# Kernel optimization log

Measured on AMD Instinct MI355X. Metric: run time of the kernel, lower is better.

The kernel has to match this reference:

```python
import jax, jax.numpy as jnp
import numpy as np
from jax import lax

LATENT = 64
NUM_EMB = 512
BETA = 0.25
DN = ('NCHW', 'OIHW', 'NCHW')


def conv(x, w, b, stride, pad):
    y = lax.conv_general_dilated(x, w, (stride, stride), [(pad, pad), (pad, pad)],
                                 dimension_numbers=DN)
    return y + b[None, :, None, None]


def tconv(x, w, b, stride, pad, opad):
    # torch ConvTranspose2d(k=3, stride, padding=pad, output_padding=opad)
    # == dilated conv with lhs_dilation=stride, padding (k-1-pad, k-1-pad+opad),
    #    spatially-flipped kernel. w is stored OIHW (out, in, kh, kw).
    k = w.shape[2]
    lo, hi = k - 1 - pad, k - 1 - pad + opad
    y = lax.conv_general_dilated(x, w[:, :, ::-1, ::-1], (1, 1), [(lo, hi), (lo, hi)],
                                 lhs_dilation=(stride, stride), dimension_numbers=DN)
    return y + b[None, :, None, None]


def vector_quantize(z, codebook):
    # z: (B, D, H, W); codebook: (K, D)
    B, D, H, W = z.shape
    flat = z.transpose(0, 2, 3, 1).reshape(-1, D)  # (BHW, D)
    d = (jnp.sum(flat ** 2, axis=1, keepdims=True)
         + jnp.sum(codebook ** 2, axis=1)
         - 2.0 * flat @ codebook.T)  # (BHW, K)
    idx = jnp.argmin(d, axis=1)
    q = codebook[idx].reshape(B, H, W, D).transpose(0, 3, 1, 2)  # (B, D, H, W)
    commitment = jnp.mean((lax.stop_gradient(q) - z) ** 2)
    codebook_loss = jnp.mean((q - lax.stop_gradient(z)) ** 2)
    loss = BETA * commitment + codebook_loss
    q_ste = z + lax.stop_gradient(q - z)  # straight-through estimator
    return q_ste, loss


def setup_inputs() -> dict:
    key = jax.random.key(0)
    ks = jax.random.split(key, 16)
    f32 = jnp.float32
    inp = {
        'x': jax.random.uniform(ks[0], (1024, 1, 50, 50), dtype=f32),
        'enc_w1': jax.random.normal(ks[1], (32, 1, 3, 3), f32) * 0.1,
        'enc_b1': jnp.zeros((32,), f32),
        'enc_w2': jax.random.normal(ks[2], (64, 32, 3, 3), f32) * 0.05,
        'enc_b2': jnp.zeros((64,), f32),
        'enc_w3': jax.random.normal(ks[3], (LATENT, 64, 1, 1), f32) * 0.1,
        'enc_b3': jnp.zeros((LATENT,), f32),
        'codebook': jax.random.uniform(ks[4], (NUM_EMB, LATENT), dtype=f32),
        'dec_w1': jax.random.normal(ks[5], (64, LATENT, 3, 3), f32) * 0.05,
        'dec_b1': jnp.zeros((64,), f32),
        'dec_w2': jax.random.normal(ks[6], (32, 64, 3, 3), f32) * 0.05,
        'dec_b2': jnp.zeros((32,), f32),
        'dec_w3': jax.random.normal(ks[7], (1, 32, 3, 3), f32) * 0.05,
        'dec_b3': jnp.zeros((1,), f32),
    }
    return inp


def reference(x, enc_w1, enc_b1, enc_w2, enc_b2, enc_w3, enc_b3, codebook,
              dec_w1, dec_b1, dec_w2, dec_b2, dec_w3, dec_b3):
    # encoder: (B,1,50,50) -> (B,LATENT,13,13)
    h = jax.nn.relu(conv(x, enc_w1, enc_b1, 2, 1))
    h = jax.nn.relu(conv(h, enc_w2, enc_b2, 2, 1))
    z = conv(h, enc_w3, enc_b3, 1, 0)
    q, vq_loss = vector_quantize(z, codebook)
    # decoder: 13 -> 25 -> 50
    h = jax.nn.relu(tconv(q, dec_w1, dec_b1, 2, 1, 0))
    h = jax.nn.relu(tconv(h, dec_w2, dec_b2, 2, 1, 1))
    x_recon = jax.nn.sigmoid(conv(h, dec_w3, dec_b3, 1, 1))
    return x_recon, vq_loss
```

## Files before the change

### kernel.cpp

```cpp
#include <hip/hip_runtime.h>
#include <math.h>


typedef __attribute__((ext_vector_type(8))) short s8v;
typedef __attribute__((ext_vector_type(4))) float f4v;
typedef __attribute__((ext_vector_type(4))) int i4v;
typedef __attribute__((ext_vector_type(4))) short s4v;
typedef __attribute__((ext_vector_type(2))) float f2v;

__device__ inline unsigned short f2bf(float f) {
    unsigned u = __builtin_bit_cast(unsigned, f);
    return (unsigned short)((u + 0x7fffu + ((u >> 16) & 1u)) >> 16);
}
__device__ inline float bf2f(unsigned short h) {
    return __builtin_bit_cast(float, ((unsigned)h) << 16);
}

__global__ __launch_bounds__(256) void k_prep_all(
        const float* __restrict__ cb,  const float* __restrict__ ew2,
        const float* __restrict__ ew3, const float* __restrict__ dw1,
        const float* __restrict__ dw2, const float* __restrict__ dw3,
        unsigned short* __restrict__ cbm, unsigned short* __restrict__ wB2n,
        unsigned short* __restrict__ wB1, unsigned short* __restrict__ wB2,
        unsigned short* __restrict__ wB3, float* __restrict__ cn,
        float* __restrict__ loss, f2v* __restrict__ wpk) {
    int i = blockIdx.x * 256 + threadIdx.x;
    if (i < 98304) {
        int j = i & 7, lane = (i >> 3) & 63;
        int kc = (i >> 9) % 6, nt = (i >> 9) / 6;
        int n = nt * 16 + (lane & 15);
        int k = kc * 32 + ((lane >> 4) << 3) + j;
        int seg = k >> 6, kk = k & 63;
        float c = cb[n * 64 + kk];
        unsigned short ch = f2bf(c);
        cbm[i] = (seg == 1) ? f2bf(c - bf2f(ch)) : ch;
    } else if (i < 153600) {
        int q = i - 98304;
        int j = q & 7, lane = (q >> 3) & 63;
        int kc = (q >> 9) % 27, nt = (q >> 9) / 27;
        int k = kc * 32 + ((lane >> 4) << 3) + j;
        int co = nt * 16 + (lane & 15);
        int part = (k < 288) ? 0 : (k < 576) ? 1 : 0;
        int kk = (k < 288) ? k : (k < 576) ? k - 288 : k - 576;
        int tap = kk >> 5, ci = kk & 31;
        float v = ew2[(co * 32 + ci) * 9 + tap];
        unsigned short hi = f2bf(v);
        wB2n[q] = part ? f2bf(v - bf2f(hi)) : hi;
    } else if (i < 219136) {
        int q = i - 153600;
        int j = q & 7, l = (q >> 3) & 63, kc = (q >> 9) & 7, nt = q >> 12;
        int n = nt * 16 + (l & 15), k = kc * 32 + (l >> 4) * 8 + j;
        int cls = n >> 6, co = n & 63, p = k >> 6, ci = k & 63;
        int jh = -1, jw = -1;
        if (cls == 0)      { if (p == 0) { jh = 1; jw = 1; } }
        else if (cls == 1) { if (p == 1) { jh = 1; jw = 0; } else if (p == 0) { jh = 1; jw = 2; } }
        else if (cls == 2) { if (p == 2) { jh = 0; jw = 1; } else if (p == 0) { jh = 2; jw = 1; } }
        else { if (p == 3) { jh = 0; jw = 0; } else if (p == 2) { jh = 0; jw = 2; }
               else if (p == 1) { jh = 2; jw = 0; } else { jh = 2; jw = 2; } }
        float v = (jh >= 0) ? dw1[((co * 64 + ci) * 3 + jh) * 3 + jw] : 0.f;
        wB1[q] = f2bf(v);
    } else if (i < 251904) {
        int q = i - 219136;
        int j = q & 7, l = (q >> 3) & 63, kc = (q >> 9) & 7, nt = q >> 12;
        int n = nt * 16 + (l & 15), k = kc * 32 + (l >> 4) * 8 + j;
        int cls = n >> 5, co = n & 31, p = k >> 6, ci = k & 63;
        int jh = -1, jw = -1;
        if (cls == 0)      { if (p == 0) { jh = 1; jw = 1; } }
        else if (cls == 1) { if (p == 1) { jh = 1; jw = 0; } else if (p == 0) { jh = 1; jw = 2; } }
        else if (cls == 2) { if (p == 2) { jh = 0; jw = 1; } else if (p == 0) { jh = 2; jw = 1; } }
        else { if (p == 3) { jh = 0; jw = 0; } else if (p == 2) { jh = 0; jw = 2; }
               else if (p == 1) { jh = 2; jw = 0; } else { jh = 2; jw = 2; } }
        float v = (jh >= 0) ? dw2[((co * 64 + ci) * 3 + jh) * 3 + jw] : 0.f;
        wB2[q] = f2bf(v);
    } else if (i < 264192) {
        int q = i - 251904;
        int j = q & 7, lane = (q >> 3) & 63;
        int kc = (q >> 9) % 6, nt = (q >> 9) / 6;
        int k = kc * 32 + ((lane >> 4) << 3) + j;
        int n = nt * 16 + (lane & 15);
        int part = (k < 64) ? 0 : (k < 128) ? 1 : 0;
        int kk = (k < 64) ? k : (k < 128) ? k - 64 : k - 128;
        float v = ew3[n * 64 + kk];
        unsigned short hi = f2bf(v);
        wB3[q] = part ? f2bf(v - bf2f(hi)) : hi;
    } else if (i < 264704) {
        int k = i - 264192;
        const float* r = cb + k * 64;
        float s = 0.f;
#pragma unroll
        for (int c = 0; c < 64; ++c) s += r[c] * r[c];
        cn[k] = s;
    } else if (i == 264704) {
        *loss = 0.f;
    } else if (i < 264849) {
        int q = i - 264705;
        int kw = q / 48, rem = q % 48, kh = rem / 16, ii = rem % 16;
        f2v w;
        w[0] = dw3[(2 * ii) * 9 + kh * 3 + kw];
        w[1] = dw3[(2 * ii + 1) * 9 + kh * 3 + kw];
        wpk[q] = w;
    }
}

__global__ __launch_bounds__(256) void k_conv1(const float* __restrict__ x,
                                               const float* __restrict__ w,
                                               const float* __restrict__ b,
                                               unsigned short* __restrict__ h1,
                                               int total) {
    __shared__ float4 wl4[72];
    float* wl = (float*)wl4;
    int tid = threadIdx.x;
    for (int t = tid; t < 288; t += 256) {
        int tap = t >> 5, co = t & 31;
        wl[t] = w[co * 9 + tap];
    }
    __syncthreads();
    int pix = blockIdx.x * 256 + tid;
    if (pix >= total) return;
    int n = pix / 625, p = pix % 625, oh = p / 25, ow = p % 25;
    const float* xp = x + (size_t)n * 2500;
    float4 a[8];
#pragma unroll
    for (int j = 0; j < 8; ++j) a[j] = ((const float4*)b)[j];
#pragma unroll
    for (int kh = 0; kh < 3; ++kh) {
        int ih = 2 * oh - 1 + kh;
        if ((unsigned)ih >= 50u) continue;
#pragma unroll
        for (int kw = 0; kw < 3; ++kw) {
            int iw = 2 * ow - 1 + kw;
            if ((unsigned)iw >= 50u) continue;
            float v = xp[ih * 50 + iw];
            int tap = kh * 3 + kw;
#pragma unroll
            for (int j = 0; j < 8; ++j) {
                float4 ww = wl4[tap * 8 + j];
                a[j].x += v * ww.x; a[j].y += v * ww.y;
                a[j].z += v * ww.z; a[j].w += v * ww.w;
            }
        }
    }
    unsigned short hi[32], lo[32];
#pragma unroll
    for (int j = 0; j < 8; ++j) {
        float vv[4] = {a[j].x, a[j].y, a[j].z, a[j].w};
#pragma unroll
        for (int e = 0; e < 4; ++e) {
            float v = fmaxf(vv[e], 0.f);
            unsigned short h = f2bf(v);
            hi[j * 4 + e] = h;
            lo[j * 4 + e] = f2bf(v - bf2f(h));
        }
    }
    i4v* op = (i4v*)(h1 + (size_t)pix * 64);
#pragma unroll
    for (int g = 0; g < 4; ++g) {
        i4v ph, pl;
#pragma unroll
        for (int e = 0; e < 4; ++e) {
            int b0 = g * 8 + e * 2;
            ph[e] = (int)((unsigned)hi[b0] | ((unsigned)hi[b0 + 1] << 16));
            pl[e] = (int)((unsigned)lo[b0] | ((unsigned)lo[b0 + 1] << 16));
        }
        op[g] = ph;
        op[4 + g] = pl;
    }
}

__global__ __launch_bounds__(256, 2) void k_enc_m(const unsigned short* __restrict__ h1,
                                                  const unsigned short* __restrict__ B2n,
                                                  const unsigned short* __restrict__ B3,
                                                  const float* __restrict__ b2,
                                                  const float* __restrict__ b3,
                                                  unsigned short* __restrict__ z, int npix) {
    __shared__ short a1[16 * 728];
    __shared__ short a2[16 * 136];
    __shared__ short czs[16 * 136];
    int tid = threadIdx.x, blk = blockIdx.x;
#pragma unroll
    for (int pass = 0; pass < 5; ++pass) {
        int u = tid + pass * 256;
        if (u < 1152) {
            int m = u / 72, rem = u - m * 72;
            int idx = rem >> 2, sub = rem & 3;
            int seg = (idx >= 9) ? 1 : 0;
            int t = idx - seg * 9;
            i4v v = (i4v){0, 0, 0, 0};
            int pix = blk * 16 + m;
            if (pix < npix) {
                int n = pix / 169, p = pix % 169, oh = p / 13, ow = p % 13;
                int ih = 2 * oh - 1 + t / 3, iw = 2 * ow - 1 + t % 3;
                if (((unsigned)ih < 25u) && ((unsigned)iw < 25u))
                    v = *(const i4v*)(h1 + (((size_t)n * 25 + ih) * 25 + iw) * 64
                                      + (seg * 4 + sub) * 8);
            }
            *(i4v*)(a1 + m * 728 + seg * 360 + t * 40 + sub * 8) = v;
        }
    }
    __syncthreads();
    int wave = tid >> 6, lane = tid & 63;
    int r = lane & 15, g = lane >> 4;
    int abase = r * 728 + g * 8;
    s8v ah[9], al[9];
#pragma unroll
    for (int t = 0; t < 9; ++t) {
        ah[t] = *(const s8v*)(a1 + abase + t * 40);
        al[t] = *(const s8v*)(a1 + abase + 360 + t * 40);
    }
    f4v acc = (f4v){0.f, 0.f, 0.f, 0.f};
#pragma unroll
    for (int kc = 0; kc < 27; ++kc) {
        s8v b = *(const s8v*)((const short*)B2n + ((size_t)((wave * 27 + kc) * 64 + lane)) * 8);
        s8v a = (kc < 9) ? ah[kc] : (kc < 18) ? ah[kc - 9] : al[kc - 18];
        acc = __builtin_amdgcn_mfma_f32_16x16x32_bf16(a, b, acc, 0, 0, 0);
    }
    {
        float bv = b2[wave * 16 + r];
        int n = wave * 16 + r;
#pragma unroll
        for (int rr = 0; rr < 4; ++rr) {
            int m = g * 4 + rr;
            float h = fmaxf(acc[rr] + bv, 0.f);
            unsigned short hh = f2bf(h);
            a2[m * 136 + n] = (short)hh;
            a2[m * 136 + 64 + n] = (short)f2bf(h - bf2f(hh));
        }
    }
    __syncthreads();
    int arow2 = r * 136 + g * 8;
    s8v zh0 = *(const s8v*)(a2 + arow2);
    s8v zh1 = *(const s8v*)(a2 + arow2 + 32);
    s8v zl0 = *(const s8v*)(a2 + arow2 + 64);
    s8v zl1 = *(const s8v*)(a2 + arow2 + 96);
    f4v acc2 = (f4v){0.f, 0.f, 0.f, 0.f};
    {
        const short* bp3 = (const short*)B3 + ((size_t)(wave * 6 * 64 + lane)) * 8;
        s8v b0 = *(const s8v*)(bp3);
        s8v b1 = *(const s8v*)(bp3 + 64 * 8);
        s8v b2f = *(const s8v*)(bp3 + 2 * 64 * 8);
        s8v b3f = *(const s8v*)(bp3 + 3 * 64 * 8);
        s8v b4 = *(const s8v*)(bp3 + 4 * 64 * 8);
        s8v b5 = *(const s8v*)(bp3 + 5 * 64 * 8);
        acc2 = __builtin_amdgcn_mfma_f32_16x16x32_bf16(zh0, b0, acc2, 0, 0, 0);
        acc2 = __builtin_amdgcn_mfma_f32_16x16x32_bf16(zh1, b1, acc2, 0, 0, 0);
        acc2 = __builtin_amdgcn_mfma_f32_16x16x32_bf16(zh0, b2f, acc2, 0, 0, 0);
        acc2 = __builtin_amdgcn_mfma_f32_16x16x32_bf16(zh1, b3f, acc2, 0, 0, 0);
        acc2 = __builtin_amdgcn_mfma_f32_16x16x32_bf16(zl0, b4, acc2, 0, 0, 0);
        acc2 = __builtin_amdgcn_mfma_f32_16x16x32_bf16(zl1, b5, acc2, 0, 0, 0);
    }
    {
        float bv = b3[wave * 16 + r];
        int n = wave * 16 + r;
#pragma unroll
        for (int rr = 0; rr < 4; ++rr) {
            int m = g * 4 + rr;
            float v = acc2[rr] + bv;
            unsigned short hh = f2bf(v);
            czs[m * 136 + n] = (short)hh;
            czs[m * 136 + 64 + n] = (short)f2bf(v - bf2f(hh));
        }
    }
    __syncthreads();
    {
        int m = tid >> 4, t = tid & 15;
        int pix = blk * 16 + m;
        if (pix < npix)
            *(i4v*)(z + (size_t)pix * 128 + t * 8) = *(i4v*)(czs + m * 136 + t * 8);
    }
}

__global__ __launch_bounds__(256, 2) void k_vq_m(const unsigned short* __restrict__ z,
                                                 const float* __restrict__ cb,
                                                 const unsigned short* __restrict__ cbm,
                                                 const float* __restrict__ cn,
                                                 unsigned short* __restrict__ q,
                                                 float* __restrict__ lpart, int npix) {
    __shared__ short a_lds[128 * 136];
    __shared__ int bkf[128];
    __shared__ float lred4[4];
    int tid = threadIdx.x, blk = blockIdx.x;
    {
        const i4v* src = (const i4v*)(z + (size_t)blk * 128 * 128);
#pragma unroll
        for (int it = 0; it < 8; ++it) {
            int L = it * 256 + tid;
            int m = L >> 4, s = L & 15;
            int pix = blk * 128 + m;
            i4v v = (i4v){0, 0, 0, 0};
            if (pix < npix) v = src[L];
            *(i4v*)(a_lds + m * 136 + s * 8) = v;
        }
    }
    __syncthreads();
    int wave = tid >> 6, lane = tid & 63;
    int arow0 = (wave * 32 + (lane & 15)) * 136 + (lane >> 4) * 8;
    int arow1 = arow0 + 16 * 136;
    s8v af00 = *(const s8v*)(a_lds + arow0);
    s8v af01 = *(const s8v*)(a_lds + arow0 + 32);
    s8v af02 = *(const s8v*)(a_lds + arow0 + 64);
    s8v af03 = *(const s8v*)(a_lds + arow0 + 96);
    s8v af10 = *(const s8v*)(a_lds + arow1);
    s8v af11 = *(const s8v*)(a_lds + arow1 + 32);
    s8v af12 = *(const s8v*)(a_lds + arow1 + 64);
    s8v af13 = *(const s8v*)(a_lds + arow1 + 96);
    float bd0[4], bd1[4];
    int bk0[4], bk1[4];
#pragma unroll
    for (int r = 0; r < 4; ++r) {
        bd0[r] = 3.4e38f; bk0[r] = 0;
        bd1[r] = 3.4e38f; bk1[r] = 0;
    }
    const s8v* bp = (const s8v*)cbm + lane;
    int ln15 = lane & 15;
    s8v bfA[6], bfB[6];
#pragma unroll
    for (int kc = 0; kc < 6; ++kc) bfA[kc] = bp[kc * 64];
    float cnA = cn[ln15];
    float cnB;
    for (int nt = 0; nt < 32; nt += 2) {
#pragma unroll
        for (int kc = 0; kc < 6; ++kc) bfB[kc] = bp[((nt + 1) * 6 + kc) * 64];
        cnB = cn[(nt + 1) * 16 + ln15];
        {
            f4v acc0 = (f4v){0.f, 0.f, 0.f, 0.f};
            f4v acc1 = (f4v){0.f, 0.f, 0.f, 0.f};
            acc0 = __builtin_amdgcn_mfma_f32_16x16x32_bf16(af00, bfA[0], acc0, 0, 0, 0);
            acc1 = __builtin_amdgcn_mfma_f32_16x16x32_bf16(af10, bfA[0], acc1, 0, 0, 0);
            acc0 = __builtin_amdgcn_mfma_f32_16x16x32_bf16(af01, bfA[1], acc0, 0, 0, 0);
            acc1 = __builtin_amdgcn_mfma_f32_16x16x32_bf16(af11, bfA[1], acc1, 0, 0, 0);
            acc0 = __builtin_amdgcn_mfma_f32_16x16x32_bf16(af00, bfA[2], acc0, 0, 0, 0);
            acc1 = __builtin_amdgcn_mfma_f32_16x16x32_bf16(af10, bfA[2], acc1, 0, 0, 0);
            acc0 = __builtin_amdgcn_mfma_f32_16x16x32_bf16(af01, bfA[3], acc0, 0, 0, 0);
            acc1 = __builtin_amdgcn_mfma_f32_16x16x32_bf16(af11, bfA[3], acc1, 0, 0, 0);
            acc0 = __builtin_amdgcn_mfma_f32_16x16x32_bf16(af02, bfA[4], acc0, 0, 0, 0);
            acc1 = __builtin_amdgcn_mfma_f32_16x16x32_bf16(af12, bfA[4], acc1, 0, 0, 0);
            acc0 = __builtin_amdgcn_mfma_f32_16x16x32_bf16(af03, bfA[5], acc0, 0, 0, 0);
            acc1 = __builtin_amdgcn_mfma_f32_16x16x32_bf16(af13, bfA[5], acc1, 0, 0, 0);
            int kcol = nt * 16 + ln15;
#pragma unroll
            for (int r = 0; r < 4; ++r) {
                float d0 = cnA - 2.f * acc0[r];
                if (d0 < bd0[r]) { bd0[r] = d0; bk0[r] = kcol; }
                float d1 = cnA - 2.f * acc1[r];
                if (d1 < bd1[r]) { bd1[r] = d1; bk1[r] = kcol; }
            }
        }
        if (nt + 2 < 32) {
#pragma unroll
            for (int kc = 0; kc < 6; ++kc) bfA[kc] = bp[((nt + 2) * 6 + kc) * 64];
            cnA = cn[(nt + 2) * 16 + ln15];
        }
        {
            f4v acc0 = (f4v){0.f, 0.f, 0.f, 0.f};
            f4v acc1 = (f4v){0.f, 0.f, 0.f, 0.f};
            acc0 = __builtin_amdgcn_mfma_f32_16x16x32_bf16(af00, bfB[0], acc0, 0, 0, 0);
            acc1 = __builtin_amdgcn_mfma_f32_16x16x32_bf16(af10, bfB[0], acc1, 0, 0, 0);
            acc0 = __builtin_amdgcn_mfma_f32_16x16x32_bf16(af01, bfB[1], acc0, 0, 0, 0);
            acc1 = __builtin_amdgcn_mfma_f32_16x16x32_bf16(af11, bfB[1], acc1, 0, 0, 0);
            acc0 = __builtin_amdgcn_mfma_f32_16x16x32_bf16(af00, bfB[2], acc0, 0, 0, 0);
            acc1 = __builtin_amdgcn_mfma_f32_16x16x32_bf16(af10, bfB[2], acc1, 0, 0, 0);
            acc0 = __builtin_amdgcn_mfma_f32_16x16x32_bf16(af01, bfB[3], acc0, 0, 0, 0);
            acc1 = __builtin_amdgcn_mfma_f32_16x16x32_bf16(af11, bfB[3], acc1, 0, 0, 0);
            acc0 = __builtin_amdgcn_mfma_f32_16x16x32_bf16(af02, bfB[4], acc0, 0, 0, 0);
            acc1 = __builtin_amdgcn_mfma_f32_16x16x32_bf16(af12, bfB[4], acc1, 0, 0, 0);
            acc0 = __builtin_amdgcn_mfma_f32_16x16x32_bf16(af03, bfB[5], acc0, 0, 0, 0);
            acc1 = __builtin_amdgcn_mfma_f32_16x16x32_bf16(af13, bfB[5], acc1, 0, 0, 0);
            int kcol = (nt + 1) * 16 + ln15;
#pragma unroll
            for (int r = 0; r < 4; ++r) {
                float d0 = cnB - 2.f * acc0[r];
                if (d0 < bd0[r]) { bd0[r] = d0; bk0[r] = kcol; }
                float d1 = cnB - 2.f * acc1[r];
                if (d1 < bd1[r]) { bd1[r] = d1; bk1[r] = kcol; }
            }
        }
    }
#pragma unroll
    for (int off = 1; off < 16; off <<= 1) {
#pragma unroll
        for (int r = 0; r < 4; ++r) {
            float od = __shfl_xor(bd0[r], off);
            int ok = __shfl_xor(bk0[r], off);
            if (od < bd0[r] || (od == bd0[r] && ok < bk0[r])) { bd0[r] = od; bk0[r] = ok; }
            od = __shfl_xor(bd1[r], off);
            ok = __shfl_xor(bk1[r], off);
            if (od < bd1[r] || (od == bd1[r] && ok < bk1[r])) { bd1[r] = od; bk1[r] = ok; }
        }
    }
    if ((lane & 15) == 0) {
#pragma unroll
        for (int r = 0; r < 4; ++r) {
            bkf[wave * 32 + (lane >> 4) * 4 + r] = bk0[r];
            bkf[wave * 32 + 16 + (lane >> 4) * 4 + r] = bk1[r];
        }
    }
    __syncthreads();
    float lsum = 0.f;
#pragma unroll
    for (int it = 0; it < 8; ++it) {
        int L = it * 256 + tid;
        int m = L >> 4, c4 = L & 15;
        int pix = blk * 128 + m;
        if (pix < npix) {
            int k0 = bkf[m];
            float4 cq = ((const float4*)cb)[(size_t)k0 * 16 + c4];
            const short* rz = a_lds + m * 136 + c4 * 4;
            s4v zh4 = *(const s4v*)rz;
            s4v zl4 = *(const s4v*)(rz + 64);
            float zx = bf2f((unsigned short)zh4[0]) + bf2f((unsigned short)zl4[0]);
            float zy = bf2f((unsigned short)zh4[1]) + bf2f((unsigned short)zl4[1]);
            float zz = bf2f((unsigned short)zh4[2]) + bf2f((unsigned short)zl4[2]);
            float zw = bf2f((unsigned short)zh4[3]) + bf2f((unsigned short)zl4[3]);
            float dx = cq.x - zx, dy = cq.y - zy, dz = cq.z - zz, dw = cq.w - zw;
            lsum += dx * dx + dy * dy + dz * dz + dw * dw;
            s4v qs;
            qs[0] = (short)f2bf(cq.x); qs[1] = (short)f2bf(cq.y);
            qs[2] = (short)f2bf(cq.z); qs[3] = (short)f2bf(cq.w);
            *(s4v*)(q + (size_t)pix * 64 + c4 * 4) = qs;
        }
    }
#pragma unroll
    for (int off = 32; off > 0; off >>= 1) lsum += __shfl_down(lsum, off);
    if (lane == 0) lred4[wave] = lsum;
    __syncthreads();
    if (tid == 0) lpart[blk] = lred4[0] + lred4[1] + lred4[2] + lred4[3];
}

__global__ __launch_bounds__(256) void k_loss(const float* __restrict__ lpart,
                                              int nblk, float* __restrict__ loss) {
    int tid = threadIdx.x;
    float s = 0.f;
    for (int i = tid; i < nblk; i += 256) s += lpart[i];
#pragma unroll
    for (int off = 32; off > 0; off >>= 1) s += __shfl_down(s, off);
    __shared__ float w4[4];
    if ((tid & 63) == 0) w4[tid >> 6] = s;
    __syncthreads();
    if (tid == 0)
        atomicAdd(loss, (w4[0] + w4[1] + w4[2] + w4[3]) * (1.25f / 11075584.f));
}

__global__ __launch_bounds__(256, 4) void k_tconv1_m(const unsigned short* __restrict__ q,
                                                     const unsigned short* __restrict__ wB,
                                                     const float* __restrict__ bias,
                                                     unsigned short* __restrict__ d1) {
    __shared__ short a_t[3 * 14 * 72];
    __shared__ short c_lds[32 * 264];
    int tid = threadIdx.x;
    int b = blockIdx.x, img = blockIdx.y;
#pragma unroll
    for (int pass = 0; pass < 2; ++pass) {
        int u = tid + pass * 256;
        if (u < 384) {
            int px = u >> 3, part = u & 7;
            int r = px >> 4, c = px & 15;
            if (c < 14) {
                i4v v = (i4v){0, 0, 0, 0};
                int grow = 2 * b + r;
                if (grow < 13 && c < 13)
                    v = *(const i4v*)(q + ((size_t)img * 169 + grow * 13 + c) * 64 + part * 8);
                *(i4v*)(a_t + (r * 14 + c) * 72 + part * 8) = v;
            }
        }
    }
    __syncthreads();
    int wave = tid >> 6, lane = tid & 63;
    int g8 = (lane >> 4) * 8;
    int qw = lane & 15;
    int qwc = (qw < 13) ? qw : 0;
    int base0 = qwc * 72;
    int base1 = (14 + qwc) * 72;
    f4v acc[2][4];
#pragma unroll
    for (int mt = 0; mt < 2; ++mt)
#pragma unroll
        for (int i = 0; i < 4; ++i) acc[mt][i] = (f4v){0.f, 0.f, 0.f, 0.f};
    float bv[4];
#pragma unroll
    for (int i = 0; i < 4; ++i) bv[i] = bias[((wave * 4 + i) * 16 + (lane & 15)) & 63];
#pragma unroll
    for (int kc = 0; kc < 8; ++kc) {
        int k0 = kc * 32 + g8;
        int p = k0 >> 6, ci0 = k0 & 63;
        int off = ((p >> 1) * 14 + (p & 1)) * 72 + ci0;
        s8v a0 = *(const s8v*)(a_t + base0 + off);
        s8v a1 = *(const s8v*)(a_t + base1 + off);
#pragma unroll
        for (int i = 0; i < 4; ++i) {
            int nt = wave * 4 + i;
            s8v bb = *(const s8v*)((const short*)wB + ((size_t)((nt * 8 + kc) * 64 + lane)) * 8);
            acc[0][i] = __builtin_amdgcn_mfma_f32_16x16x32_bf16(a0, bb, acc[0][i], 0, 0, 0);
            acc[1][i] = __builtin_amdgcn_mfma_f32_16x16x32_bf16(a1, bb, acc[1][i], 0, 0, 0);
        }
    }
#pragma unroll
    for (int mt = 0; mt < 2; ++mt)
#pragma unroll
        for (int i = 0; i < 4; ++i) {
            int n = (wave * 4 + i) * 16 + (lane & 15);
#pragma unroll
            for (int r2 = 0; r2 < 4; ++r2) {
                int m = mt * 16 + (lane >> 4) * 4 + r2;
                float v = fmaxf(acc[mt][i][r2] + bv[i], 0.f);
                c_lds[m * 264 + n] = (short)f2bf(v);
            }
        }
    __syncthreads();
#pragma unroll
    for (int pass = 0; pass < 4; ++pass) {
        int ch = tid + pass * 256;
        int m = ch >> 5, cpart = ch & 31;
        int qwO = m & 15, qr = m >> 4;
        if (qwO >= 13) continue;
        int qm = 2 * b + qr;
        if (qm >= 13) continue;
        int cls = cpart >> 3, co8 = (cpart & 7) * 8;
        int oh = 2 * qm + (cls >> 1), ow = 2 * qwO + (cls & 1);
        if (oh >= 25 || ow >= 25) continue;
        i4v val = *(i4v*)(c_lds + m * 264 + cls * 64 + co8);
        *(i4v*)(d1 + (((size_t)img * 25 + oh) * 25 + ow) * 64 + co8) = val;
    }
}

__global__ __launch_bounds__(256, 4) void k_tconv2_m(const unsigned short* __restrict__ d1,
                                                     const unsigned short* __restrict__ wB,
                                                     const float* __restrict__ bias,
                                                     unsigned short* __restrict__ d2) {
    __shared__ short a_t[3 * 26 * 72];
    __shared__ short c_lds[64 * 136];
    int tid = threadIdx.x;
    int b = blockIdx.x, img = blockIdx.y;
#pragma unroll
    for (int pass = 0; pass < 3; ++pass) {
        int u = tid + pass * 256;
        int px = u >> 3, part = u & 7;
        int r = px >> 5, c = px & 31;
        if (c < 26) {
            i4v v = (i4v){0, 0, 0, 0};
            int grow = 2 * b + r;
            if (grow < 25 && c < 25)
                v = *(const i4v*)(d1 + (((size_t)img * 25 + grow) * 25 + c) * 64 + part * 8);
            *(i4v*)(a_t + (r * 26 + c) * 72 + part * 8) = v;
        }
    }
    __syncthreads();
    int wave = tid >> 6, lane = tid & 63;
    int g8 = (lane >> 4) * 8;
    int qwA = lane & 15;
    int qwB = 16 + (lane & 15);
    int qBc = (qwB < 25) ? qwB : 0;
    int base0 = qwA * 72;
    int base1 = qBc * 72;
    int base2 = (26 + qwA) * 72;
    int base3 = (26 + qBc) * 72;
    f4v acc[4][2];
#pragma unroll
    for (int mt = 0; mt < 4; ++mt)
#pragma unroll
        for (int i = 0; i < 2; ++i) acc[mt][i] = (f4v){0.f, 0.f, 0.f, 0.f};
    float bv[2];
#pragma unroll
    for (int i = 0; i < 2; ++i) bv[i] = bias[((wave * 2 + i) * 16 + (lane & 15)) & 31];
#pragma unroll
    for (int kc = 0; kc < 8; ++kc) {
        int k0 = kc * 32 + g8;
        int p = k0 >> 6, ci0 = k0 & 63;
        int off = ((p >> 1) * 26 + (p & 1)) * 72 + ci0;
        s8v a0 = *(const s8v*)(a_t + base0 + off);
        s8v a1 = *(const s8v*)(a_t + base1 + off);
        s8v a2 = *(const s8v*)(a_t + base2 + off);
        s8v a3 = *(const s8v*)(a_t + base3 + off);
#pragma unroll
        for (int i = 0; i < 2; ++i) {
            int nt = wave * 2 + i;
            s8v bb = *(const s8v*)((const short*)wB + ((size_t)((nt * 8 + kc) * 64 + lane)) * 8);
            acc[0][i] = __builtin_amdgcn_mfma_f32_16x16x32_bf16(a0, bb, acc[0][i], 0, 0, 0);
            acc[1][i] = __builtin_amdgcn_mfma_f32_16x16x32_bf16(a1, bb, acc[1][i], 0, 0, 0);
            acc[2][i] = __builtin_amdgcn_mfma_f32_16x16x32_bf16(a2, bb, acc[2][i], 0, 0, 0);
            acc[3][i] = __builtin_amdgcn_mfma_f32_16x16x32_bf16(a3, bb, acc[3][i], 0, 0, 0);
        }
    }
#pragma unroll
    for (int mt = 0; mt < 4; ++mt)
#pragma unroll
        for (int i = 0; i < 2; ++i) {
            int n = (wave * 2 + i) * 16 + (lane & 15);
#pragma unroll
            for (int r2 = 0; r2 < 4; ++r2) {
                int m = mt * 16 + (lane >> 4) * 4 + r2;
                float v = fmaxf(acc[mt][i][r2] + bv[i], 0.f);
                c_lds[m * 136 + n] = (short)f2bf(v);
            }
        }
    __syncthreads();
#pragma unroll
    for (int pass = 0; pass < 4; ++pass) {
        int ch = tid + pass * 256;
        int m = ch >> 4, cpart = ch & 15;
        int qwO = m & 31, qr = m >> 5;
        if (qwO >= 25) continue;
        int qm = 2 * b + qr;
        if (qm >= 25) continue;
        int cls = cpart >> 2, co8 = (cpart & 3) * 8;
        int oh = 2 * qm + (cls >> 1), ow = 2 * qwO + (cls & 1);
        i4v val = *(i4v*)(c_lds + m * 136 + cls * 32 + co8);
        *(i4v*)(d2 + (((size_t)img * 50 + oh) * 50 + ow) * 32 + co8) = val;
    }
}

__global__ __launch_bounds__(256, 2) void k_convf(const unsigned short* __restrict__ in,
                                                  const f2v* __restrict__ wpk,
                                                  const float* __restrict__ b,
                                                  float* __restrict__ out) {
    int img = blockIdx.x;
    int t = threadIdx.x;
    if (t >= 250) return;
    int strip = t / 50, col = t % 50;
    int r0 = strip * 10;
    const unsigned short* base = in + (size_t)img * 80000;
    f2v acc[10];
#pragma unroll
    for (int i = 0; i < 10; ++i) acc[i] = (f2v){0.f, 0.f};
    for (int dx = -1; dx <= 1; ++dx) {
        int ic = col + dx;
        if ((unsigned)ic >= 50u) continue;
        int kw = dx + 1;
        const f2v* wp = wpk + kw * 48;
        f2v w2r[3][16];
#pragma unroll
        for (int kh = 0; kh < 3; ++kh)
#pragma unroll
            for (int i = 0; i < 16; ++i) w2r[kh][i] = wp[kh * 16 + i];
#pragma unroll
        for (int rr = -1; rr <= 10; ++rr) {
            int ih = r0 + rr;
            if ((unsigned)ih >= 50u) continue;
            const i4v* px = (const i4v*)(base + ((size_t)ih * 50 + ic) * 32);
#pragma unroll
            for (int c8 = 0; c8 < 4; ++c8) {
                i4v u = px[c8];
#pragma unroll
                for (int e = 0; e < 4; ++e) {
                    unsigned uu = (unsigned)u[e];
                    f2v x;
                    x[0] = __builtin_bit_cast(float, uu << 16);
                    x[1] = __builtin_bit_cast(float, uu & 0xffff0000u);
                    int i = c8 * 4 + e;
                    if (rr - 1 >= 0 && rr - 1 <= 9) acc[rr - 1] += x * w2r[2][i];
                    if (rr >= 0 && rr <= 9)         acc[rr]     += x * w2r[1][i];
                    if (rr + 1 >= 0 && rr + 1 <= 9) acc[rr + 1] += x * w2r[0][i];
                }
            }
        }
    }
    float b0 = b[0];
    float* op = out + (size_t)img * 2500 + (size_t)r0 * 50 + col;
#pragma unroll
    for (int i = 0; i < 10; ++i) {
        float v = acc[i][0] + acc[i][1] + b0;
        op[(size_t)i * 50] = 1.f / (1.f + expf(-v));
    }
}

extern "C" void kernel_launch(void* const* d_in, const int* in_sizes, int n_in,
                              void* d_out, int out_size, void* d_ws, size_t ws_size,
                              hipStream_t stream) {
    const float* x   = (const float*)d_in[0];
    const float* ew1 = (const float*)d_in[1];
    const float* eb1 = (const float*)d_in[2];
    const float* ew2 = (const float*)d_in[3];
    const float* eb2 = (const float*)d_in[4];
    const float* ew3 = (const float*)d_in[5];
    const float* eb3 = (const float*)d_in[6];
    const float* cb  = (const float*)d_in[7];
    const float* dw1 = (const float*)d_in[8];
    const float* db1 = (const float*)d_in[9];
    const float* dw2 = (const float*)d_in[10];
    const float* db2 = (const float*)d_in[11];
    const float* dw3 = (const float*)d_in[12];
    const float* db3 = (const float*)d_in[13];
    float* out = (float*)d_out;
    float* loss = out + 2560000;

    float* ws = (float*)d_ws;
    float* cn = ws;
    unsigned short* wB1  = (unsigned short*)(ws + 512);
    unsigned short* wB2  = (unsigned short*)(ws + 33280);
    unsigned short* wB2n = (unsigned short*)(ws + 49664);
    unsigned short* wB3  = (unsigned short*)(ws + 77312);
    unsigned short* cbm  = (unsigned short*)(ws + 83456);
    float* lpart = ws + 132608;
    f2v* wpk = (f2v*)(ws + 133968);
    const size_t tw_floats = 134256;

    const int B = 1024;
    const size_t A_per = 40000, B_per = 20000;
    size_t avail = (ws_size / 4 > tw_floats) ? ws_size / 4 - tw_floats : 0;
    int BC = (int)(avail / (A_per + B_per));
    if (BC > B) BC = B;
    if (BC < 1) BC = 1;
    float* regA = ws + tw_floats;
    float* regB = regA + (size_t)BC * A_per;

    k_prep_all<<<1035, 256, 0, stream>>>(cb, ew2, ew3, dw1, dw2, dw3,
                                         cbm, wB2n, wB1, wB2, wB3, cn, loss, wpk);

    for (int n0 = 0; n0 < B; n0 += BC) {
        int bc = (B - n0 < BC) ? (B - n0) : BC;
        const float* xch = x + (size_t)n0 * 2500;

        int t1 = bc * 625;
        unsigned short* h1p = (unsigned short*)regA;
        k_conv1<<<(t1 + 255) / 256, 256, 0, stream>>>(xch, ew1, eb1, h1p, t1);

        int npix = bc * 169;
        unsigned short* zp = (unsigned short*)regB;
        k_enc_m<<<(npix + 15) / 16, 256, 0, stream>>>(h1p, wB2n, wB3, eb2, eb3, zp, npix);

        unsigned short* qb = (unsigned short*)regA;
        int nblk = (npix + 127) / 128;
        k_vq_m<<<nblk, 256, 0, stream>>>(zp, cb, cbm, cn, qb, lpart, npix);

        k_loss<<<1, 256, 0, stream>>>(lpart, nblk, loss);

        unsigned short* d1 = (unsigned short*)regB;
        k_tconv1_m<<<dim3(7, bc), 256, 0, stream>>>(qb, wB1, db1, d1);

        unsigned short* d2 = (unsigned short*)regA;
        k_tconv2_m<<<dim3(13, bc), 256, 0, stream>>>(d1, wB2, db2, d2);

        k_convf<<<bc, 256, 0, stream>>>(d2, wpk, db3, out + (size_t)n0 * 2500);
    }
}
```

Before: 433.6 us.

## Stage final conv input strips in LDS and split image across five blocks

The final 3x3 conv (32->1 channels, sigmoid) now launches five blocks per image. Each block cooperatively loads a 12-row halo strip of bf16 activations into padded shared memory and computes two output rows per thread, where before one block per image had each thread stream a 10-row column directly from global memory. This increases parallelism and cuts register pressure from ten accumulators to two. In exchange, each thread now runs only 2 outputs on 4 input rows, so halo rows are loaded twice across adjacent blocks, and a barrier plus about 43 KB of LDS per block is added.

```diff
diff --git a/kernel.cpp b/kernel.cpp
--- a/kernel.cpp
+++ b/kernel.cpp
@@ -612,15 +612,29 @@
                                                   const f2v* __restrict__ wpk,
                                                   const float* __restrict__ b,
                                                   float* __restrict__ out) {
-    int img = blockIdx.x;
-    int t = threadIdx.x;
-    if (t >= 250) return;
-    int strip = t / 50, col = t % 50;
+    __shared__ short lds[12 * 50 * 36];
+    int strip = blockIdx.x, img = blockIdx.y;
     int r0 = strip * 10;
-    const unsigned short* base = in + (size_t)img * 80000;
-    f2v acc[10];
-#pragma unroll
-    for (int i = 0; i < 10; ++i) acc[i] = (f2v){0.f, 0.f};
+    int tid = threadIdx.x;
+#pragma unroll
+    for (int pass = 0; pass < 10; ++pass) {
+        int u = tid + pass * 256;
+        if (u < 2400) {
+            int px = u >> 2, chunk = u & 3;
+            int row = px / 50, col = px - row * 50;
+            int gr = r0 - 1 + row;
+            i4v v = (i4v){0, 0, 0, 0};
+            if ((unsigned)gr < 50u)
+                v = *(const i4v*)(in + (((size_t)img * 50 + gr) * 50 + col) * 32 + chunk * 8);
+            *(i4v*)(lds + (row * 50 + col) * 36 + chunk * 8) = v;
+        }
+    }
+    __syncthreads();
+    if (tid >= 250) return;
+    int orow = tid / 50, col = tid - orow * 50;
+    int lbase = 2 * orow;
+    f2v acc0 = (f2v){0.f, 0.f};
+    f2v acc1 = (f2v){0.f, 0.f};
     for (int dx = -1; dx <= 1; ++dx) {
         int ic = col + dx;
         if ((unsigned)ic >= 50u) continue;
@@ -632,13 +646,11 @@
 #pragma unroll
             for (int i = 0; i < 16; ++i) w2r[kh][i] = wp[kh * 16 + i];
 #pragma unroll
-        for (int rr = -1; rr <= 10; ++rr) {
-            int ih = r0 + rr;
-            if ((unsigned)ih >= 50u) continue;
-            const i4v* px = (const i4v*)(base + ((size_t)ih * 50 + ic) * 32);
+        for (int lr = 0; lr < 4; ++lr) {
+            const short* px = lds + ((lbase + lr) * 50 + ic) * 36;
 #pragma unroll
             for (int c8 = 0; c8 < 4; ++c8) {
-                i4v u = px[c8];
+                i4v u = *(const i4v*)(px + c8 * 8);
 #pragma unroll
                 for (int e = 0; e < 4; ++e) {
                     unsigned uu = (unsigned)u[e];
@@ -646,20 +658,18 @@
                     x[0] = __builtin_bit_cast(float, uu << 16);
                     x[1] = __builtin_bit_cast(float, uu & 0xffff0000u);
                     int i = c8 * 4 + e;
-                    if (rr - 1 >= 0 && rr - 1 <= 9) acc[rr - 1] += x * w2r[2][i];
-                    if (rr >= 0 && rr <= 9)         acc[rr]     += x * w2r[1][i];
-                    if (rr + 1 >= 0 && rr + 1 <= 9) acc[rr + 1] += x * w2r[0][i];
+                    if (lr <= 2) acc0 += x * w2r[lr][i];
+                    if (lr >= 1) acc1 += x * w2r[lr - 1][i];
                 }
             }
         }
     }
     float b0 = b[0];
-    float* op = out + (size_t)img * 2500 + (size_t)r0 * 50 + col;
-#pragma unroll
-    for (int i = 0; i < 10; ++i) {
-        float v = acc[i][0] + acc[i][1] + b0;
-        op[(size_t)i * 50] = 1.f / (1.f + expf(-v));
-    }
+    float* op = out + (size_t)img * 2500 + (size_t)(r0 + 2 * orow) * 50 + col;
+    float v0 = acc0[0] + acc0[1] + b0;
+    float v1 = acc1[0] + acc1[1] + b0;
+    op[0]  = 1.f / (1.f + expf(-v0));
+    op[50] = 1.f / (1.f + expf(-v1));
 }
 
 extern "C" void kernel_launch(void* const* d_in, const int* in_sizes, int n_in,
@@ -729,6 +739,6 @@
         unsigned short* d2 = (unsigned short*)regA;
         k_tconv2_m<<<dim3(13, bc), 256, 0, stream>>>(d1, wB2, db2, d2);
 
-        k_convf<<<bc, 256, 0, stream>>>(d2, wpk, db3, out + (size_t)n0 * 2500);
-    }
-}
+        k_convf<<<dim3(5, bc), 256, 0, stream>>>(d2, wpk, db3, out + (size_t)n0 * 2500);
+    }
+}
```

Result: slower. 477.9 us (+10.2%).
